# Performance work log

Hardware: AMD Instinct MI355X
Metric: run time of the kernel (lower is better)

Reference implementation:

```python
import jax, jax.numpy as jnp
import numpy as np

N, CIN, COUT = 8, 256, 512
HEADS, DK, DV = 8, 256, 256
MAP = 32          # H = W = map_size
KS, PAD = 3, 1
DKH = DK // HEADS  # 32
DVH = DV // HEADS  # 32
CONV_OUT = COUT - DV  # 256


def conv2d(x, w, b, stride=1, padding=0):
    out = jax.lax.conv_general_dilated(
        x, w, (stride, stride), [(padding, padding), (padding, padding)],
        dimension_numbers=("NCHW", "OIHW", "NCHW"))
    return out + b[None, :, None, None]


def rel_to_abs(x):
    # x: [B, G, L, 2L-1] relative logits -> [B, G, L, L] absolute (skewing trick)
    B, G, L, _ = x.shape
    x = jnp.pad(x, ((0, 0), (0, 0), (0, 0), (0, 1)))          # [B,G,L,2L]
    flat = x.reshape(B, G, L * 2 * L)
    flat = jnp.pad(flat, ((0, 0), (0, 0), (0, L - 1)))
    return flat.reshape(B, G, L + 1, 2 * L - 1)[:, :, :L, L - 1:]


def setup_inputs() -> dict:
    key = jax.random.key(0)
    ks = jax.random.split(key, 16)
    def w(k, shape, fan_in):
        return jax.random.normal(k, shape, jnp.float32) * (fan_in ** -0.5)
    inp = {
        "x": jax.random.normal(ks[0], (N, CIN, MAP, MAP), jnp.float32),
        "conv_w": w(ks[1], (CONV_OUT, CIN, KS, KS), CIN * KS * KS),
        "conv_b": jnp.zeros((CONV_OUT,), jnp.float32),
        "q_w": w(ks[2], (DK, CIN, KS, KS), CIN * KS * KS),
        "q_b": jnp.zeros((DK,), jnp.float32),
        "k_w": w(ks[3], (DK, CIN, KS, KS), CIN * KS * KS),
        "k_b": jnp.zeros((DK,), jnp.float32),
        "v_w": w(ks[4], (DV, CIN, KS, KS), CIN * KS * KS),
        "v_b": jnp.zeros((DV,), jnp.float32),
        "attn_w": w(ks[5], (DV, DV, 1, 1), DV),
        "attn_b": jnp.zeros((DV,), jnp.float32),
        "width_mat": jax.random.normal(ks[6], (2 * MAP - 1, DKH), jnp.float32) * (DKH ** -0.5),
        "height_mat": jax.random.normal(ks[7], (2 * MAP - 1, DKH), jnp.float32) * (DKH ** -0.5),
    }
    return inp


def reference(x, conv_w, conv_b, q_w, q_b, k_w, k_b, v_w, v_b,
              attn_w, attn_b, width_mat, height_mat):
    conv_maps = conv2d(x, conv_w, conv_b, 1, PAD)            # [N, 256, H, W]
    H = W = MAP
    q = conv2d(x, q_w, q_b, 1, PAD).reshape(N, HEADS, DKH, H, W)
    k = conv2d(x, k_w, k_b, 1, PAD).reshape(N, HEADS, DKH, H, W)
    v = conv2d(x, v_w, v_b, 1, PAD).reshape(N, HEADS, DVH, H, W)

    qf = q.reshape(N, HEADS, DKH, H * W)
    kf = k.reshape(N, HEADS, DKH, H * W)
    vf = v.reshape(N, HEADS, DVH, H * W)
    logits = jnp.einsum("nhdq,nhdk->nhqk", qf, kf)           # [N,h,HW,HW]

    qp = q.transpose(0, 1, 3, 4, 2)                          # [N,h,H,W,dkh]
    # width relative logits: depends on (hq, wq, wk), broadcast over hk
    rel_w = jnp.einsum("nhyxd,rd->nhyxr", qp, width_mat)     # [N,h,H,W,2W-1]
    abs_w = rel_to_abs(rel_w.reshape(N, HEADS * H, W, 2 * W - 1)
                       ).reshape(N, HEADS, H, W, W)          # [N,h,hq,wq,wk]
    # height relative logits: depends on (wq, hq, hk), broadcast over wk
    rel_h = jnp.einsum("nhyxd,rd->nhxyr", qp, height_mat)    # [N,h,W,H,2H-1]
    abs_h = rel_to_abs(rel_h.reshape(N, HEADS * W, H, 2 * H - 1)
                       ).reshape(N, HEADS, W, H, H)          # [N,h,wq,hq,hk]

    w_bias = abs_w[:, :, :, :, None, :]                      # [N,h,hq,wq,1,wk]
    h_bias = abs_h.transpose(0, 1, 3, 2, 4)[..., None]       # [N,h,hq,wq,hk,1]
    logits = (logits.reshape(N, HEADS, H, W, H, W) + h_bias + w_bias
              ).reshape(N, HEADS, H * W, H * W)
    logits = logits * (DKH ** -0.5)

    weights = jax.nn.softmax(logits, axis=-1)
    attn = jnp.einsum("nhqk,nhdk->nhqd", weights, vf)        # [N,h,HW,dvh]
    # faithful to torch .view quirk: row-major reshape [HW,dvh] -> [dvh,H,W]
    attn_maps = attn.reshape(N, HEADS * DVH, H, W)
    attn_maps = conv2d(attn_maps, attn_w, attn_b, 1, 0)
    return jnp.concatenate([conv_maps, attn_maps], axis=1)
```

## Files before the change

kernel.cpp:

```cpp
#include <hip/hip_runtime.h>
#include <hip/hip_bf16.h>


typedef __attribute__((ext_vector_type(8))) __bf16 bf16x8;
typedef __attribute__((ext_vector_type(4))) float f32x4;
typedef unsigned short u16;
typedef unsigned int u32;
typedef __attribute__((ext_vector_type(8))) u16 u16x8;

#define GLD(gp, lp) __builtin_amdgcn_global_load_lds( \
    (const __attribute__((address_space(1))) u32*)(gp), \
    (__attribute__((address_space(3))) u32*)(lp), 16, 0, 0)

static __device__ __forceinline__ u16 f2bf(float f) {
  u32 u = __builtin_bit_cast(u32, f);
  u += 0x7fffu + ((u >> 16) & 1u);
  return (u16)(u >> 16);
}
static __device__ __forceinline__ float bf2f(u16 h) {
  return __builtin_bit_cast(float, (u32)h << 16);
}

__global__ __launch_bounds__(256) void k_cast_w(
    const float* __restrict__ conv_w, const float* __restrict__ q_w,
    const float* __restrict__ k_w, const float* __restrict__ v_w,
    const float* __restrict__ attn_w, u16* __restrict__ W9, u16* __restrict__ W1) {
  __shared__ float t[2304];
  int row = blockIdx.x;
  const float* src = row < 256 ? conv_w : row < 512 ? q_w : row < 768 ? k_w : v_w;
  const float* sr = src + (row & 255) * 2304;
#pragma unroll
  for (int i = threadIdx.x; i < 2304; i += 256) t[i] = sr[i];
  __syncthreads();
  u16* dr = W9 + row * 2304;
#pragma unroll
  for (int i = threadIdx.x; i < 2304; i += 256) {
    int t9 = i >> 8, c = i & 255;
    dr[i] = f2bf(t[c * 9 + t9]);
  }
  if (row < 256) W1[row * 256 + threadIdx.x] = f2bf(attn_w[row * 256 + threadIdx.x]);
}

__global__ void k_xT(const float* __restrict__ x, u16* __restrict__ xT,
                     u16* __restrict__ zpage) {
  if (blockIdx.x == 0 && threadIdx.x < 512) zpage[threadIdx.x] = 0;
  __shared__ float t[32][33];
  int b = blockIdx.x;
  int sb = b & 31, cb = (b >> 5) & 7, n = b >> 8;
  int s0 = sb << 5, c0 = cb << 5;
  int ls = threadIdx.x & 31, lc = threadIdx.x >> 5;
#pragma unroll
  for (int i = 0; i < 4; ++i) {
    int c = lc + i * 8;
    t[c][ls] = x[(((n << 8) + c0 + c) << 10) + s0 + ls];
  }
  __syncthreads();
#pragma unroll
  for (int i = 0; i < 4; ++i) {
    int s = lc + i * 8;
    xT[(((n << 10) + s0 + s) << 8) + c0 + ls] = f2bf(t[ls][s]);
  }
}

__global__ __launch_bounds__(512) void k_gemm_conv(
    const u16* __restrict__ A, const u16* __restrict__ xT, const u16* __restrict__ zpage,
    float* __restrict__ out,
    u16* __restrict__ qb, u16* __restrict__ kb, u16* __restrict__ vb,
    const float* __restrict__ conv_b, const float* __restrict__ q_b,
    const float* __restrict__ k_b, const float* __restrict__ v_b) {
  __shared__ u16 As[2][16384];
  __shared__ u16 Bs[2][8192];
  f32x4 acc[4][4] = {};
  const int tid = threadIdx.x;
  const int wave = tid >> 6, lane = tid & 63;
  const int wr = wave >> 1, wc = wave & 1;
  const int lr = lane & 15, lk = lane >> 4;
  const int srow = lane >> 3;
  const int swz = 8 * ((lane & 7) ^ (srow & 7));
  const int bm = blockIdx.x, bn = blockIdx.y;

  int bn_y[2], bn_x[2], bn_base[2];
#pragma unroll
  for (int r = 0; r < 2; ++r) {
    int col = bn * 128 + r * 64 + wave * 8 + srow;
    int n = col >> 10, s = col & 1023;
    bn_y[r] = s >> 5;
    bn_x[r] = s & 31;
    bn_base[r] = n << 10;
  }
  const u16* a_src[4];
#pragma unroll
  for (int a = 0; a < 4; ++a)
    a_src[a] = A + (bm * 256 + a * 64 + wave * 8 + srow) * 2304 + swz;

  auto stage = [&](int buf, int t) {
    int k0 = t << 6;
    int t9 = k0 >> 8;
    int dy = t9 / 3 - 1, dx = t9 - (t9 / 3) * 3 - 1;
    int c0 = k0 & 255;
#pragma unroll
    for (int a = 0; a < 4; ++a)
      GLD(a_src[a] + k0, &As[buf][a * 4096 + wave * 512]);
#pragma unroll
    for (int r = 0; r < 2; ++r) {
      int sy = bn_y[r] + dy, sx = bn_x[r] + dx;
      bool ok = ((u32)sy < 32u) && ((u32)sx < 32u);
      const u16* src = ok ? (xT + ((bn_base[r] + (sy << 5) + sx) << 8) + c0 + swz)
                          : (zpage + swz);
      GLD(src, &Bs[buf][r * 4096 + wave * 512]);
    }
  };

  const int rswz = lr & 7;
  const int arow = (wr * 64 + lr) * 64;
  const int brow = (wc * 64 + lr) * 64;

  auto compute = [&](int buf) {
#pragma unroll
    for (int kk = 0; kk < 2; ++kk) {
      const int cswz = (((kk << 2) | lk) ^ rswz) << 3;
      bf16x8 af[4], bv[4];
#pragma unroll
      for (int m = 0; m < 4; ++m)
        af[m] = *(const bf16x8*)&As[buf][arow + m * 1024 + cswz];
#pragma unroll
      for (int n = 0; n < 4; ++n)
        bv[n] = *(const bf16x8*)&Bs[buf][brow + n * 1024 + cswz];
      __builtin_amdgcn_s_setprio(1);
#pragma unroll
      for (int m = 0; m < 4; ++m)
#pragma unroll
        for (int n = 0; n < 4; ++n)
          acc[m][n] = __builtin_amdgcn_mfma_f32_16x16x32_bf16(af[m], bv[n], acc[m][n], 0, 0, 0);
      __builtin_amdgcn_s_setprio(0);
    }
  };

  stage(0, 0);
  stage(1, 1);
  for (int t = 0; t < 35; ++t) {
    asm volatile("s_waitcnt vmcnt(6)" ::: "memory");
    __builtin_amdgcn_s_barrier();
    compute(t & 1);
    __builtin_amdgcn_s_barrier();
    if (t + 2 < 36) stage(t & 1, t + 2);
  }
  asm volatile("s_waitcnt vmcnt(0)" ::: "memory");
  __builtin_amdgcn_s_barrier();
  compute(35 & 1);

  const int row0 = bm * 256 + wr * 64 + lk * 4;
  const int col0 = bn * 128 + wc * 64 + lr;
#pragma unroll
  for (int m = 0; m < 4; ++m) {
#pragma unroll
    for (int n = 0; n < 4; ++n) {
      int col = col0 + n * 16;
      int nn = col >> 10, s = col & 1023;
#pragma unroll
      for (int j = 0; j < 4; ++j) {
        int c = row0 + m * 16 + j;
        float v = acc[m][n][j];
        if (c < 256) {
          out[((nn << 9) + c) * 1024 + s] = v + conv_b[c];
        } else if (c < 512) {
          int cc = c - 256;
          qb[((((nn << 3) + (cc >> 5)) << 10) + s) * 32 + (cc & 31)] = f2bf(v + q_b[cc]);
        } else if (c < 768) {
          int cc = c - 512;
          kb[((((nn << 3) + (cc >> 5)) << 10) + s) * 32 + (cc & 31)] = f2bf(v + k_b[cc]);
        } else {
          int cc = c - 768;
          vb[((nn << 8) + cc) * 1024 + s] = f2bf(v + v_b[cc]);
        }
      }
    }
  }
}

__global__ __launch_bounds__(256) void k_bias(const u16* __restrict__ qb,
                                              const float* __restrict__ wm,
                                              const float* __restrict__ hm,
                                              float* __restrict__ Bw, float* __restrict__ Bh) {
  __shared__ float wl[63 * 36], hl[63 * 36];
  for (int i = threadIdx.x; i < 2016; i += 256) {
    int r = i >> 5, c = i & 31;
    wl[r * 36 + c] = wm[i];
    hl[r * 36 + c] = hm[i];
  }
  __syncthreads();
  int pos = blockIdx.x * blockDim.x + threadIdx.x;
  int s = pos & 1023;
  int y = s >> 5, xx = s & 31;
  float q[32];
  const u16x8* q8 = (const u16x8*)(qb + pos * 32);
#pragma unroll
  for (int v = 0; v < 4; ++v) {
    u16x8 w = q8[v];
#pragma unroll
    for (int e = 0; e < 8; ++e) q[v * 8 + e] = bf2f(w[e]);
  }
  float* bwo = Bw + pos * 32;
  float* bho = Bh + pos * 32;
#pragma unroll 4
  for (int r = 0; r < 32; ++r) {
    const f32x4* wr = (const f32x4*)&wl[(r - xx + 31) * 36];
    const f32x4* hr = (const f32x4*)&hl[(r - y + 31) * 36];
    float aw = 0.f, ah = 0.f;
#pragma unroll
    for (int i = 0; i < 8; ++i) {
      f32x4 wv = wr[i], hv = hr[i];
#pragma unroll
      for (int e = 0; e < 4; ++e) {
        float qd = q[i * 4 + e];
        aw += qd * wv[e];
        ah += qd * hv[e];
      }
    }
    bwo[r] = aw;
    bho[r] = ah;
  }
}

__global__ __launch_bounds__(256) void k_attn(
    const u16* __restrict__ qb, const u16* __restrict__ kb, const u16* __restrict__ vb,
    const float* __restrict__ Bw, const float* __restrict__ Bh, u16* __restrict__ AMT) {
  __shared__ u16 Pl[4][16 * 72];
  const int wave = threadIdx.x >> 6, lane = threadIdx.x & 63;
  const int task = blockIdx.x * 4 + wave;
  const int nh = task >> 6, qg = task & 63;
  const int n = nh >> 3, h = nh & 7;
  const int qbase = qg << 4;
  const int lr = lane & 15, lg = lane >> 4;

  bf16x8 aq = *(const bf16x8*)&qb[((nh << 10) + qbase + lr) * 32 + lg * 8];

  float Bwr[2][4];
#pragma unroll
  for (int p = 0; p < 2; ++p)
#pragma unroll
    for (int j = 0; j < 4; ++j)
      Bwr[p][j] = Bw[((nh << 10) + qbase + lg * 4 + j) * 32 + p * 16 + lr];

  float mrow[4] = {-1e30f, -1e30f, -1e30f, -1e30f};
  float lrow[4] = {0.f, 0.f, 0.f, 0.f};
  f32x4 o[2] = {};
  u16* pl = Pl[wave];

  for (int kt = 0; kt < 16; ++kt) {
    f32x4 zero = {0.f, 0.f, 0.f, 0.f};
    f32x4 sf_[4];
#pragma unroll
    for (int f = 0; f < 4; ++f) {
      bf16x8 bk = *(const bf16x8*)&kb[((nh << 10) + (kt << 6) + f * 16 + lr) * 32 + lg * 8];
      sf_[f] = __builtin_amdgcn_mfma_f32_16x16x32_bf16(aq, bk, zero, 0, 0, 0);
    }
    float Bhr[2][4];
#pragma unroll
    for (int p = 0; p < 2; ++p)
#pragma unroll
      for (int j = 0; j < 4; ++j)
        Bhr[p][j] = Bh[((nh << 10) + qbase + lg * 4 + j) * 32 + (kt << 1) + p];
    float tv[4][4];
#pragma unroll
    for (int f = 0; f < 4; ++f)
#pragma unroll
      for (int j = 0; j < 4; ++j)
        tv[f][j] = (sf_[f][j] + Bhr[f >> 1][j] + Bwr[f & 1][j]) * 0.17677669529663687f;

    float pv[4][4], sf[4];
#pragma unroll
    for (int j = 0; j < 4; ++j) {
      float vmax = fmaxf(fmaxf(tv[0][j], tv[1][j]), fmaxf(tv[2][j], tv[3][j]));
#pragma unroll
      for (int d = 1; d < 16; d <<= 1) vmax = fmaxf(vmax, __shfl_xor(vmax, d, 64));
      float mn = fmaxf(mrow[j], vmax);
      sf[j] = __expf(mrow[j] - mn);
      mrow[j] = mn;
      float sum = 0.f;
#pragma unroll
      for (int f = 0; f < 4; ++f) {
        float e = __expf(tv[f][j] - mn);
        pv[f][j] = e;
        sum += e;
      }
#pragma unroll
      for (int d = 1; d < 16; d <<= 1) sum += __shfl_xor(sum, d, 64);
      lrow[j] = lrow[j] * sf[j] + sum;
    }
#pragma unroll
    for (int dn = 0; dn < 2; ++dn)
#pragma unroll
      for (int j = 0; j < 4; ++j) o[dn][j] *= sf[j];

#pragma unroll
    for (int f = 0; f < 4; ++f)
#pragma unroll
      for (int j = 0; j < 4; ++j)
        pl[(lg * 4 + j) * 72 + f * 16 + lr] = f2bf(pv[f][j]);
    asm volatile("s_waitcnt lgkmcnt(0)" ::: "memory");
    __builtin_amdgcn_sched_barrier(0);
    bf16x8 pa0 = *(const bf16x8*)&pl[lr * 72 + lg * 8];
    bf16x8 pa1 = *(const bf16x8*)&pl[lr * 72 + 32 + lg * 8];
#pragma unroll
    for (int dn = 0; dn < 2; ++dn) {
      bf16x8 bv0 = *(const bf16x8*)&vb[((n << 8) + (h << 5) + dn * 16 + lr) * 1024 + (kt << 6) + lg * 8];
      o[dn] = __builtin_amdgcn_mfma_f32_16x16x32_bf16(pa0, bv0, o[dn], 0, 0, 0);
      bf16x8 bv1 = *(const bf16x8*)&vb[((n << 8) + (h << 5) + dn * 16 + lr) * 1024 + (kt << 6) + 32 + lg * 8];
      o[dn] = __builtin_amdgcn_mfma_f32_16x16x32_bf16(pa1, bv1, o[dn], 0, 0, 0);
    }
  }
#pragma unroll
  for (int dn = 0; dn < 2; ++dn)
#pragma unroll
    for (int j = 0; j < 4; ++j) {
      int q = qbase + lg * 4 + j;
      int d = dn * 16 + lr;
      float v = o[dn][j] / lrow[j];
      AMT[((n << 10) + ((q & 31) << 5) + d) * 256 + (h << 5) + (q >> 5)] = f2bf(v);
    }
}

static __device__ __forceinline__ void gemm_core(const u16* __restrict__ A,
                                                 const u16* __restrict__ B, int K,
                                                 u16* As, u16* Bs, f32x4 acc[4][4]) {
  const int tid = threadIdx.x;
  const int wave = tid >> 6, lane = tid & 63;
  const int wr = wave >> 1, wc = wave & 1;
  const int lr = lane & 15, lk = lane >> 4;
  const int srow = lane >> 3;
  const int scol = (lane & 7) << 3;
  const int bm = blockIdx.x, bn = blockIdx.y;
  for (int k0 = 0; k0 < K; k0 += 64) {
#pragma unroll
    for (int i = 0; i < 4; ++i) {
      int seg = i * 4 + wave;
      GLD(A + (bm * 128 + seg * 8 + srow) * K + k0 + scol, As + seg * 512);
      GLD(B + (bn * 128 + seg * 8 + srow) * K + k0 + scol, Bs + seg * 512);
    }
    __syncthreads();
#pragma unroll
    for (int kk = 0; kk < 2; ++kk) {
      bf16x8 af[4], bv[4];
#pragma unroll
      for (int m = 0; m < 4; ++m)
        af[m] = *(const bf16x8*)&As[(wr * 64 + m * 16 + lr) * 64 + kk * 32 + lk * 8];
#pragma unroll
      for (int n = 0; n < 4; ++n)
        bv[n] = *(const bf16x8*)&Bs[(wc * 64 + n * 16 + lr) * 64 + kk * 32 + lk * 8];
#pragma unroll
      for (int m = 0; m < 4; ++m)
#pragma unroll
        for (int n = 0; n < 4; ++n)
          acc[m][n] = __builtin_amdgcn_mfma_f32_16x16x32_bf16(af[m], bv[n], acc[m][n], 0, 0, 0);
    }
    __syncthreads();
  }
}

__global__ __launch_bounds__(256) void k_gemm_out(
    const u16* __restrict__ A, const u16* __restrict__ B, float* __restrict__ out,
    const float* __restrict__ attn_b) {
  __shared__ u16 As[8192], Bs[8192];
  f32x4 acc[4][4] = {};
  gemm_core(A, B, 256, As, Bs, acc);
  const int tid = threadIdx.x;
  const int wave = tid >> 6, lane = tid & 63;
  const int wr = wave >> 1, wc = wave & 1;
  const int lr = lane & 15, lk = lane >> 4;
  const int row0 = blockIdx.x * 128 + wr * 64 + lk * 4;
  const int col0 = blockIdx.y * 128 + wc * 64 + lr;
#pragma unroll
  for (int m = 0; m < 4; ++m) {
#pragma unroll
    for (int n = 0; n < 4; ++n) {
      int col = col0 + n * 16;
      int nn = col >> 10, s = col & 1023;
#pragma unroll
      for (int j = 0; j < 4; ++j) {
        int c = row0 + m * 16 + j;
        out[((nn << 9) + 256 + c) * 1024 + s] = acc[m][n][j] + attn_b[c];
      }
    }
  }
}

extern "C" void kernel_launch(void* const* d_in, const int* in_sizes, int n_in,
                              void* d_out, int out_size, void* d_ws, size_t ws_size,
                              hipStream_t stream) {
  const float* x      = (const float*)d_in[0];
  const float* conv_w = (const float*)d_in[1];
  const float* conv_b = (const float*)d_in[2];
  const float* q_w    = (const float*)d_in[3];
  const float* q_b    = (const float*)d_in[4];
  const float* k_w    = (const float*)d_in[5];
  const float* k_b    = (const float*)d_in[6];
  const float* v_w    = (const float*)d_in[7];
  const float* v_b    = (const float*)d_in[8];
  const float* attn_w = (const float*)d_in[9];
  const float* attn_b = (const float*)d_in[10];
  const float* wm     = (const float*)d_in[11];
  const float* hm     = (const float*)d_in[12];
  float* out = (float*)d_out;
  char* ws = (char*)d_ws;

  u16*   W9   = (u16*)(ws + 0);
  u16*   W1   = (u16*)(ws + 4718592);
  u16*   xT   = (u16*)(ws + 4849664);
  u16*   zpg  = (u16*)(ws + 9043968);
  u16*   qbf  = (u16*)(ws + 9044992);
  u16*   kbf  = (u16*)(ws + 13239296);
  u16*   vbf  = (u16*)(ws + 17433600);
  float* Bw   = (float*)(ws + 21627904);
  float* Bh   = (float*)(ws + 30016512);
  u16*   AMT  = (u16*)(ws + 38405120);

  hipLaunchKernelGGL(k_cast_w, dim3(1024), dim3(256), 0, stream,
                     conv_w, q_w, k_w, v_w, attn_w, W9, W1);
  hipLaunchKernelGGL(k_xT, dim3(2048), dim3(256), 0, stream, x, xT, zpg);
  hipLaunchKernelGGL(k_gemm_conv, dim3(4, 64), dim3(512), 0, stream,
                     W9, xT, zpg, out, qbf, kbf, vbf, conv_b, q_b, k_b, v_b);
  hipLaunchKernelGGL(k_bias, dim3(256), dim3(256), 0, stream, qbf, wm, hm, Bw, Bh);
  hipLaunchKernelGGL(k_attn, dim3(1024), dim3(256), 0, stream, qbf, kbf, vbf, Bw, Bh, AMT);
  hipLaunchKernelGGL(k_gemm_out, dim3(2, 64), dim3(256), 0, stream, W1, AMT, out, attn_b);
}
```

Before: 253.3 us.

## Software-pipeline PV matmul in attention and halve output GEMM N-tile

```diff
diff --git a/kernel.cpp b/kernel.cpp
--- a/kernel.cpp
+++ b/kernel.cpp
@@ -225,7 +225,7 @@
 __global__ __launch_bounds__(256) void k_attn(
     const u16* __restrict__ qb, const u16* __restrict__ kb, const u16* __restrict__ vb,
     const float* __restrict__ Bw, const float* __restrict__ Bh, u16* __restrict__ AMT) {
-  __shared__ u16 Pl[4][16 * 72];
+  __shared__ u16 Pl[4][2][16 * 72];
   const int wave = threadIdx.x >> 6, lane = threadIdx.x & 63;
   const int task = blockIdx.x * 4 + wave;
   const int nh = task >> 6, qg = task & 63;
@@ -244,10 +244,14 @@
 
   float mrow[4] = {-1e30f, -1e30f, -1e30f, -1e30f};
   float lrow[4] = {0.f, 0.f, 0.f, 0.f};
+  float sfp[4] = {1.f, 1.f, 1.f, 1.f};
   f32x4 o[2] = {};
-  u16* pl = Pl[wave];
+  u16* plw = &Pl[wave][0][0];
+  const int vrow0 = ((n << 8) + (h << 5) + lr) * 1024;
+  const int vrow1 = ((n << 8) + (h << 5) + 16 + lr) * 1024;
 
   for (int kt = 0; kt < 16; ++kt) {
+    const int cur = (kt & 1) * 1152, prv = ((kt & 1) ^ 1) * 1152;
     f32x4 zero = {0.f, 0.f, 0.f, 0.f};
     f32x4 sf_[4];
 #pragma unroll
@@ -257,10 +261,11 @@
     }
     float Bhr[2][4];
 #pragma unroll
-    for (int p = 0; p < 2; ++p)
-#pragma unroll
-      for (int j = 0; j < 4; ++j)
-        Bhr[p][j] = Bh[((nh << 10) + qbase + lg * 4 + j) * 32 + (kt << 1) + p];
+    for (int j = 0; j < 4; ++j) {
+      float2 bh2 = *(const float2*)&Bh[((nh << 10) + qbase + lg * 4 + j) * 32 + (kt << 1)];
+      Bhr[0][j] = bh2.x;
+      Bhr[1][j] = bh2.y;
+    }
     float tv[4][4];
 #pragma unroll
     for (int f = 0; f < 4; ++f)
@@ -288,28 +293,57 @@
       for (int d = 1; d < 16; d <<= 1) sum += __shfl_xor(sum, d, 64);
       lrow[j] = lrow[j] * sf[j] + sum;
     }
-#pragma unroll
-    for (int dn = 0; dn < 2; ++dn)
-#pragma unroll
-      for (int j = 0; j < 4; ++j) o[dn][j] *= sf[j];
+
+    if (kt > 0) {
+      asm volatile("s_waitcnt lgkmcnt(0)" ::: "memory");
+      __builtin_amdgcn_sched_barrier(0);
+      bf16x8 pa0 = *(const bf16x8*)&plw[prv + lr * 72 + lg * 8];
+      bf16x8 pa1 = *(const bf16x8*)&plw[prv + lr * 72 + 32 + lg * 8];
+#pragma unroll
+      for (int dn = 0; dn < 2; ++dn)
+#pragma unroll
+        for (int j = 0; j < 4; ++j) o[dn][j] *= sfp[j];
+      const int kv = (kt - 1) << 6;
+      bf16x8 bv00 = *(const bf16x8*)&vb[vrow0 + kv + lg * 8];
+      bf16x8 bv01 = *(const bf16x8*)&vb[vrow0 + kv + 32 + lg * 8];
+      bf16x8 bv10 = *(const bf16x8*)&vb[vrow1 + kv + lg * 8];
+      bf16x8 bv11 = *(const bf16x8*)&vb[vrow1 + kv + 32 + lg * 8];
+      o[0] = __builtin_amdgcn_mfma_f32_16x16x32_bf16(pa0, bv00, o[0], 0, 0, 0);
+      o[0] = __builtin_amdgcn_mfma_f32_16x16x32_bf16(pa1, bv01, o[0], 0, 0, 0);
+      o[1] = __builtin_amdgcn_mfma_f32_16x16x32_bf16(pa0, bv10, o[1], 0, 0, 0);
+      o[1] = __builtin_amdgcn_mfma_f32_16x16x32_bf16(pa1, bv11, o[1], 0, 0, 0);
+    }
 
 #pragma unroll
     for (int f = 0; f < 4; ++f)
 #pragma unroll
       for (int j = 0; j < 4; ++j)
-        pl[(lg * 4 + j) * 72 + f * 16 + lr] = f2bf(pv[f][j]);
+        plw[cur + (lg * 4 + j) * 72 + f * 16 + lr] = f2bf(pv[f][j]);
+#pragma unroll
+    for (int j = 0; j < 4; ++j) sfp[j] = sf[j];
+  }
+
+  {
     asm volatile("s_waitcnt lgkmcnt(0)" ::: "memory");
     __builtin_amdgcn_sched_barrier(0);
-    bf16x8 pa0 = *(const bf16x8*)&pl[lr * 72 + lg * 8];
-    bf16x8 pa1 = *(const bf16x8*)&pl[lr * 72 + 32 + lg * 8];
-#pragma unroll
-    for (int dn = 0; dn < 2; ++dn) {
-      bf16x8 bv0 = *(const bf16x8*)&vb[((n << 8) + (h << 5) + dn * 16 + lr) * 1024 + (kt << 6) + lg * 8];
-      o[dn] = __builtin_amdgcn_mfma_f32_16x16x32_bf16(pa0, bv0, o[dn], 0, 0, 0);
-      bf16x8 bv1 = *(const bf16x8*)&vb[((n << 8) + (h << 5) + dn * 16 + lr) * 1024 + (kt << 6) + 32 + lg * 8];
-      o[dn] = __builtin_amdgcn_mfma_f32_16x16x32_bf16(pa1, bv1, o[dn], 0, 0, 0);
-    }
-  }
+    const int prv = 1152;
+    bf16x8 pa0 = *(const bf16x8*)&plw[prv + lr * 72 + lg * 8];
+    bf16x8 pa1 = *(const bf16x8*)&plw[prv + lr * 72 + 32 + lg * 8];
+#pragma unroll
+    for (int dn = 0; dn < 2; ++dn)
+#pragma unroll
+      for (int j = 0; j < 4; ++j) o[dn][j] *= sfp[j];
+    const int kv = 15 << 6;
+    bf16x8 bv00 = *(const bf16x8*)&vb[vrow0 + kv + lg * 8];
+    bf16x8 bv01 = *(const bf16x8*)&vb[vrow0 + kv + 32 + lg * 8];
+    bf16x8 bv10 = *(const bf16x8*)&vb[vrow1 + kv + lg * 8];
+    bf16x8 bv11 = *(const bf16x8*)&vb[vrow1 + kv + 32 + lg * 8];
+    o[0] = __builtin_amdgcn_mfma_f32_16x16x32_bf16(pa0, bv00, o[0], 0, 0, 0);
+    o[0] = __builtin_amdgcn_mfma_f32_16x16x32_bf16(pa1, bv01, o[0], 0, 0, 0);
+    o[1] = __builtin_amdgcn_mfma_f32_16x16x32_bf16(pa0, bv10, o[1], 0, 0, 0);
+    o[1] = __builtin_amdgcn_mfma_f32_16x16x32_bf16(pa1, bv11, o[1], 0, 0, 0);
+  }
+
 #pragma unroll
   for (int dn = 0; dn < 2; ++dn)
 #pragma unroll
@@ -321,9 +355,11 @@
     }
 }
 
-static __device__ __forceinline__ void gemm_core(const u16* __restrict__ A,
-                                                 const u16* __restrict__ B, int K,
-                                                 u16* As, u16* Bs, f32x4 acc[4][4]) {
+__global__ __launch_bounds__(256) void k_gemm_out(
+    const u16* __restrict__ A, const u16* __restrict__ B, float* __restrict__ out,
+    const float* __restrict__ attn_b) {
+  __shared__ u16 As[16384], Bs[8192];
+  f32x4 acc[4][2] = {};
   const int tid = threadIdx.x;
   const int wave = tid >> 6, lane = tid & 63;
   const int wr = wave >> 1, wc = wave & 1;
@@ -331,49 +367,41 @@
   const int srow = lane >> 3;
   const int scol = (lane & 7) << 3;
   const int bm = blockIdx.x, bn = blockIdx.y;
-  for (int k0 = 0; k0 < K; k0 += 64) {
+  for (int k0 = 0; k0 < 256; k0 += 64) {
 #pragma unroll
     for (int i = 0; i < 4; ++i) {
       int seg = i * 4 + wave;
-      GLD(A + (bm * 128 + seg * 8 + srow) * K + k0 + scol, As + seg * 512);
-      GLD(B + (bn * 128 + seg * 8 + srow) * K + k0 + scol, Bs + seg * 512);
+      GLD(A + (bm * 128 + seg * 8 + srow) * 256 + k0 + scol, As + seg * 512);
+    }
+#pragma unroll
+    for (int i = 0; i < 2; ++i) {
+      int seg = i * 4 + wave;
+      GLD(B + (bn * 64 + seg * 8 + srow) * 256 + k0 + scol, Bs + seg * 512);
     }
     __syncthreads();
 #pragma unroll
     for (int kk = 0; kk < 2; ++kk) {
-      bf16x8 af[4], bv[4];
+      bf16x8 af[4], bv[2];
 #pragma unroll
       for (int m = 0; m < 4; ++m)
         af[m] = *(const bf16x8*)&As[(wr * 64 + m * 16 + lr) * 64 + kk * 32 + lk * 8];
 #pragma unroll
-      for (int n = 0; n < 4; ++n)
-        bv[n] = *(const bf16x8*)&Bs[(wc * 64 + n * 16 + lr) * 64 + kk * 32 + lk * 8];
+      for (int n = 0; n < 2; ++n)
+        bv[n] = *(const bf16x8*)&Bs[(wc * 32 + n * 16 + lr) * 64 + kk * 32 + lk * 8];
 #pragma unroll
       for (int m = 0; m < 4; ++m)
 #pragma unroll
-        for (int n = 0; n < 4; ++n)
+        for (int n = 0; n < 2; ++n)
           acc[m][n] = __builtin_amdgcn_mfma_f32_16x16x32_bf16(af[m], bv[n], acc[m][n], 0, 0, 0);
     }
     __syncthreads();
   }
-}
-
-__global__ __launch_bounds__(256) void k_gemm_out(
-    const u16* __restrict__ A, const u16* __restrict__ B, float* __restrict__ out,
-    const float* __restrict__ attn_b) {
-  __shared__ u16 As[8192], Bs[8192];
-  f32x4 acc[4][4] = {};
-  gemm_core(A, B, 256, As, Bs, acc);
-  const int tid = threadIdx.x;
-  const int wave = tid >> 6, lane = tid & 63;
-  const int wr = wave >> 1, wc = wave & 1;
-  const int lr = lane & 15, lk = lane >> 4;
-  const int row0 = blockIdx.x * 128 + wr * 64 + lk * 4;
-  const int col0 = blockIdx.y * 128 + wc * 64 + lr;
+  const int row0 = bm * 128 + wr * 64 + lk * 4;
+  const int col0 = bn * 64 + wc * 32 + lr;
 #pragma unroll
   for (int m = 0; m < 4; ++m) {
 #pragma unroll
-    for (int n = 0; n < 4; ++n) {
+    for (int n = 0; n < 2; ++n) {
       int col = col0 + n * 16;
       int nn = col >> 10, s = col & 1023;
 #pragma unroll
@@ -422,5 +450,5 @@
                      W9, xT, zpg, out, qbf, kbf, vbf, conv_b, q_b, k_b, v_b);
   hipLaunchKernelGGL(k_bias, dim3(256), dim3(256), 0, stream, qbf, wm, hm, Bw, Bh);
   hipLaunchKernelGGL(k_attn, dim3(1024), dim3(256), 0, stream, qbf, kbf, vbf, Bw, Bh, AMT);
-  hipLaunchKernelGGL(k_gemm_out, dim3(2, 64), dim3(256), 0, stream, W1, AMT, out, attn_b);
-}
+  hipLaunchKernelGGL(k_gemm_out, dim3(2, 128), dim3(256), 0, stream, W1, AMT, out, attn_b);
+}
```

Measured after the change: 248.9 us. Within noise of the previous version (-1.7%).
